# Performance work log

Hardware: AMD Instinct MI355X
Metric: run time of the kernel (lower is better)

The kernel has to match this reference:

```python
import jax, jax.numpy as jnp
import numpy as np

B, L, H, A, M, E, R = 4, 1024, 1024, 16, 128, 32, 992
EMB, BLK, C = 768, 64, 97


def setup_inputs() -> dict:
    key = jax.random.key(0)
    ks = jax.random.split(key, 8)
    return {
        'seq_lhs': jax.random.normal(ks[0], (B, L, H), jnp.float32),
        'ent_lhs': jax.random.normal(ks[1], (B, M, H), jnp.float32),
        'ent_to_seq_attn': jax.random.uniform(ks[2], (B, A, M, L), jnp.float32),
        'mention_entity_ids': jax.random.randint(ks[3], (B, M), 0, E, jnp.int32),
        'hts': jax.random.randint(ks[4], (B, R, 2), 0, E, jnp.int32),
        'head_W': jax.random.normal(ks[5], (2 * H, EMB), jnp.float32) * 0.02,
        'head_b': jnp.zeros((EMB,), jnp.float32),
        'tail_W': jax.random.normal(ks[6], (2 * H, EMB), jnp.float32) * 0.02,
        'tail_b': jnp.zeros((EMB,), jnp.float32),
        'bil_W': jax.random.normal(ks[7], (EMB * BLK, C), jnp.float32) * 0.02,
        'bil_b': jnp.zeros((C,), jnp.float32),
    }


def _pool_doc(seq, ents, attn, ids, ht):
    # seq [L,H], ents [M,H], attn [A,M,L], ids [M], ht [R,2]
    counts = jax.ops.segment_sum(jnp.ones((M,), seq.dtype), ids, num_segments=E)  # [E]
    nz = counts > 0
    # stable segment logsumexp over mentions of each entity (matches torch.logsumexp;
    # single-mention entities reduce to the raw embedding, empty entities -> zeros)
    mx = jax.ops.segment_max(ents, ids, num_segments=E)              # [E,H]
    mx = jnp.where(nz[:, None], mx, 0.0)
    s = jax.ops.segment_sum(jnp.exp(ents - mx[ids]), ids, num_segments=E)
    s = jnp.where(nz[:, None], s, 1.0)
    ent_emb = jnp.where(nz[:, None], mx + jnp.log(s), 0.0)           # [E,H]
    # mean of mention->seq attention per entity (empty -> zeros)
    attn_m = jnp.transpose(attn, (1, 0, 2))                          # [M,A,L]
    asum = jax.ops.segment_sum(attn_m, ids, num_segments=E)          # [E,A,L]
    ent_attn = jnp.where(nz[:, None, None], asum / jnp.maximum(counts, 1.0)[:, None, None], 0.0)
    # gather head/tail entities for each pair
    hs, ts = ent_emb[ht[:, 0]], ent_emb[ht[:, 1]]                    # [R,H]
    ha, ta = ent_attn[ht[:, 0]], ent_attn[ht[:, 1]]                  # [R,A,L]
    w = (ha * ta).mean(axis=1)                                       # [R,L]
    w = w / (w.sum(axis=1, keepdims=True) + 1e-5)
    rel = jnp.einsum('ld,rl->rd', seq, w)                            # [R,H]
    return hs, ts, rel


def reference(seq_lhs, ent_lhs, ent_to_seq_attn, mention_entity_ids, hts,
              head_W, head_b, tail_W, tail_b, bil_W, bil_b):
    hs, ts, rel = jax.vmap(_pool_doc)(seq_lhs, ent_lhs, ent_to_seq_attn,
                                      mention_entity_ids, hts)
    hs = hs.reshape(-1, H)
    ts = ts.reshape(-1, H)
    rel = rel.reshape(-1, H)
    hs = jnp.tanh(jnp.concatenate([hs, rel], axis=1) @ head_W + head_b)  # [N,EMB]
    ts = jnp.tanh(jnp.concatenate([ts, rel], axis=1) @ tail_W + tail_b)
    b1 = hs.reshape(-1, EMB // BLK, BLK)
    b2 = ts.reshape(-1, EMB // BLK, BLK)
    bl = (b1[:, :, :, None] * b2[:, :, None, :]).reshape(-1, EMB * BLK)  # [N,EMB*BLK]
    return bl @ bil_W + bil_b                                            # [N,C]
```

## Files before the change

### kernel.cpp

```cpp
#include <hip/hip_runtime.h>
#include <hip/hip_bf16.h>
#include <math.h>

constexpr int cB   = 4;
constexpr int cL   = 1024;
constexpr int cH   = 1024;
constexpr int cA   = 16;
constexpr int cM   = 128;
constexpr int cE   = 32;
constexpr int cR   = 992;
constexpr int cEMB = 768;
constexpr int cC   = 97;
constexpr int cN   = cB * cR;
constexpr int cNG  = 8;

typedef unsigned short ushort;
typedef __attribute__((ext_vector_type(4))) unsigned short ushort4v;
typedef __attribute__((ext_vector_type(8))) short short8;
typedef __attribute__((ext_vector_type(4))) float float4v;

static __device__ inline float bf2f(ushort u) {
    unsigned v = ((unsigned)u) << 16;
    float f;
    __builtin_memcpy(&f, &v, 4);
    return f;
}
static __device__ inline ushort f2bf(float f) {
    unsigned u;
    __builtin_memcpy(&u, &f, 4);
    unsigned r = (u + 0x7FFFu + ((u >> 16) & 1u)) >> 16;
    return (ushort)r;
}

static __device__ inline void gld16(const ushort* src, ushort* dstbase) {
    __builtin_amdgcn_global_load_lds(
        (const __attribute__((address_space(1))) unsigned int*)src,
        (__attribute__((address_space(3))) unsigned int*)dstbase, 16, 0, 0);
}

__global__ void tr_bf16_k(const float* __restrict__ src, ushort* __restrict__ dst,
                          int R, int C, int Cp) {
    int z = blockIdx.z;
    int r0 = blockIdx.x * 32, c0 = blockIdx.y * 32;
    int tx = threadIdx.x & 31, ty = threadIdx.x >> 5;
    __shared__ float tile[32][33];
    for (int p = 0; p < 4; p++) {
        int r = r0 + ty + p * 8, c = c0 + tx;
        tile[ty + p * 8][tx] = (r < R && c < C) ? src[((size_t)z * R + r) * C + c] : 0.f;
    }
    __syncthreads();
    for (int p = 0; p < 4; p++) {
        int c = c0 + ty + p * 8, r = r0 + tx;
        if (c < Cp && r < R)
            dst[((size_t)z * Cp + c) * R + r] = f2bf(tile[tx][ty + p * 8]);
    }
}

__global__ void tr_ht_k(const float* __restrict__ Wh, const float* __restrict__ Wt,
                        ushort* __restrict__ WTh, ushort* __restrict__ WTt) {
    const float* src = blockIdx.z ? Wt : Wh;
    ushort* dst = blockIdx.z ? WTt : WTh;
    int r0 = blockIdx.x * 32, c0 = blockIdx.y * 32;
    int tx = threadIdx.x & 31, ty = threadIdx.x >> 5;
    __shared__ float tile[32][33];
    for (int p = 0; p < 4; p++) {
        int r = r0 + ty + p * 8, c = c0 + tx;
        tile[ty + p * 8][tx] = src[(size_t)r * cEMB + c];
    }
    __syncthreads();
    for (int p = 0; p < 4; p++) {
        int c = c0 + ty + p * 8, r = r0 + tx;
        dst[(size_t)c * (2 * cH) + r] = f2bf(tile[tx][ty + p * 8]);
    }
}

__global__ void wf_build_k(const float* __restrict__ W, ushort* __restrict__ Wf) {
    const int si = blockIdx.x;
    const int tid = threadIdx.x;
    __shared__ ushort sWb[64 * 136];
    for (int idx = tid; idx < 64 * 128; idx += 256) {
        int r = idx >> 7, c = idx & 127;
        float v = (c < cC) ? W[((size_t)si * 64 + r) * cC + c] : 0.f;
        sWb[r * 136 + c] = f2bf(v);
    }
    __syncthreads();
#pragma unroll
    for (int p = 0; p < 4; p++) {
        int e = tid + p * 256;
        int f = e >> 6, lane = e & 63;
        int g = lane >> 4, col = lane & 15;
        int khalf = f >> 3, ct = f & 7;
        int jb = khalf * 32 + g * 8;
        int c = ct * 16 + col;
        short8 v;
#pragma unroll
        for (int jj = 0; jj < 8; jj++) v[jj] = (short)sWb[(jb + jj) * 136 + c];
        *(short8*)&Wf[(((size_t)si * 16 + f) * 64 + lane) * 8] = v;
    }
}

__global__ void ent_pool_k(const float* __restrict__ ent_lhs, const int* __restrict__ ids,
                           ushort* __restrict__ ent_emb, int* __restrict__ counts) {
    int e = blockIdx.x, b = blockIdx.y;
    __shared__ int sid[cM];
    int tid = threadIdx.x;
    if (tid < cM) sid[tid] = ids[b * cM + tid];
    __syncthreads();
    int cnt = 0;
    for (int m = 0; m < cM; m++) cnt += (sid[m] == e) ? 1 : 0;
    if (blockIdx.z == 0 && tid == 0) counts[b * cE + e] = cnt;
    int h = blockIdx.z * 256 + tid;
    {
        float mx = -1e30f;
        for (int m = 0; m < cM; m++)
            if (sid[m] == e) mx = fmaxf(mx, ent_lhs[(size_t)(b * cM + m) * cH + h]);
        float s = 0.f;
        for (int m = 0; m < cM; m++)
            if (sid[m] == e) s += __expf(ent_lhs[(size_t)(b * cM + m) * cH + h] - mx);
        ent_emb[(size_t)(b * cE + e) * cH + h] = f2bf((cnt > 0) ? (mx + __logf(s)) : 0.f);
    }
}

__global__ void ent_attn_k(const float* __restrict__ attn, const int* __restrict__ ids,
                           const int* __restrict__ counts, ushort* __restrict__ ent_attn) {
    int ba = blockIdx.x;
    int b = ba / cA, a = ba % cA;
    int tid = threadIdx.x;
    int l = blockIdx.y * 256 + tid;
    __shared__ int sid[cM];
    __shared__ int scnt[cE];
    __shared__ float sacc[256 * 33];
    if (tid < cM) sid[tid] = ids[b * cM + tid];
    if (tid < cE) scnt[tid] = counts[b * cE + tid];
    float* acc = &sacc[tid * 33];
    for (int e2 = 0; e2 < cE; e2++) acc[e2] = 0.f;
    __syncthreads();
    const float* ap = attn + ((size_t)(b * cA + a) * cM) * cL + l;
    for (int m = 0; m < cM; m++) acc[sid[m]] += ap[(size_t)m * cL];
    for (int e2 = 0; e2 < cE; e2++) {
        ent_attn[((size_t)(b * cE + e2) * cA + a) * cL + l] =
            f2bf(acc[e2] / (float)max(scnt[e2], 1));
    }
}

__global__ void w_k(const ushort* __restrict__ ent_attn, const int* __restrict__ hts,
                    ushort* __restrict__ w) {
    int nr = blockIdx.x;
    int b = nr / cR;
    int he = hts[nr * 2 + 0], te = hts[nr * 2 + 1];
    int tid = threadIdx.x;
    int l0 = tid * 4;
    const ushort* ha = ent_attn + ((size_t)(b * cE + he) * cA) * cL + l0;
    const ushort* ta = ent_attn + ((size_t)(b * cE + te) * cA) * cL + l0;
    float v[4] = {0.f, 0.f, 0.f, 0.f};
#pragma unroll
    for (int a = 0; a < cA; a++) {
        ushort4v hv = *(const ushort4v*)&ha[(size_t)a * cL];
        ushort4v tv = *(const ushort4v*)&ta[(size_t)a * cL];
#pragma unroll
        for (int i = 0; i < 4; i++) v[i] += bf2f(hv[i]) * bf2f(tv[i]);
    }
    float psum = 0.f;
#pragma unroll
    for (int i = 0; i < 4; i++) { v[i] *= (1.0f / cA); psum += v[i]; }
    for (int off = 32; off > 0; off >>= 1) psum += __shfl_down(psum, off, 64);
    __shared__ float red[4];
    if ((tid & 63) == 0) red[tid >> 6] = psum;
    __syncthreads();
    float tot = red[0] + red[1] + red[2] + red[3];
    float inv = 1.0f / (tot + 1e-5f);
    ushort4v o;
#pragma unroll
    for (int i = 0; i < 4; i++) o[i] = f2bf(v[i] * inv);
    *(ushort4v*)&w[(size_t)nr * cL + l0] = o;
}

__global__ __launch_bounds__(256) void
rel_mfma2_k(const ushort* __restrict__ wbf, const ushort* __restrict__ seqT,
            ushort* __restrict__ relbf) {
    const int b = blockIdx.z;
    const int h0 = blockIdx.x * 128, r0 = blockIdx.y * 64;
    const int tid = threadIdx.x, lane = tid & 63, wv = tid >> 6;
    const int col = lane & 15, g4 = lane >> 4;
    const int wr = wv >> 1, wc = wv & 1;

    __shared__ ushort sA[2][64 * 64];
    __shared__ ushort sB[2][128 * 64];

    const int lr = lane >> 3;
    const int swz = (lane & 7) ^ lr;

    const int ra0 = wv * 8 + lr, ra1 = ra0 + 32;
    const ushort* a0p = wbf + ((size_t)b * cR + min(r0 + ra0, cR - 1)) * cL + swz * 8;
    const ushort* a1p = wbf + ((size_t)b * cR + min(r0 + ra1, cR - 1)) * cL + swz * 8;
    const ushort* bptr[4];
#pragma unroll
    for (int p = 0; p < 4; p++)
        bptr[p] = seqT + ((size_t)b * cH + h0 + p * 32 + wv * 8 + lr) * cL + swz * 8;

    float4v acc[2][4];
#pragma unroll
    for (int mt = 0; mt < 2; mt++)
#pragma unroll
        for (int ct = 0; ct < 4; ct++) acc[mt][ct] = (float4v){0.f, 0.f, 0.f, 0.f};

#define REL_STAGE(kt, buf) {                                                   \
        gld16(a0p + (kt), &sA[buf][wv * 512]);                                 \
        gld16(a1p + (kt), &sA[buf][(4 + wv) * 512]);                           \
        _Pragma("unroll")                                                      \
        for (int p = 0; p < 4; p++)                                            \
            gld16(bptr[p] + (kt), &sB[buf][(p * 4 + wv) * 512]);               \
    }

    REL_STAGE(0, 0);
    __syncthreads();
    int cur = 0;
    for (int kt = 0; kt < cL; kt += 64) {
        if (kt + 64 < cL) REL_STAGE(kt + 64, cur ^ 1);
#pragma unroll
        for (int k0 = 0; k0 < 64; k0 += 32) {
            short8 av[2];
#pragma unroll
            for (int mt = 0; mt < 2; mt++) {
                int ra = wr * 32 + mt * 16 + col;
                int sg = ((k0 >> 3) + g4) ^ (ra & 7);
                av[mt] = *(const short8*)&sA[cur][ra * 64 + sg * 8];
            }
#pragma unroll
            for (int ct = 0; ct < 4; ct++) {
                int rb = wc * 64 + ct * 16 + col;
                int sg = ((k0 >> 3) + g4) ^ (rb & 7);
                short8 bv = *(const short8*)&sB[cur][rb * 64 + sg * 8];
#pragma unroll
                for (int mt = 0; mt < 2; mt++)
                    acc[mt][ct] = __builtin_amdgcn_mfma_f32_16x16x32_bf16(
                        av[mt], bv, acc[mt][ct], 0, 0, 0);
            }
        }
        __syncthreads();
        cur ^= 1;
    }
#undef REL_STAGE

#pragma unroll
    for (int mt = 0; mt < 2; mt++) {
#pragma unroll
        for (int ct = 0; ct < 4; ct++) {
            int h = h0 + wc * 64 + ct * 16 + col;
            int rowb = r0 + wr * 32 + mt * 16 + g4 * 4;
#pragma unroll
            for (int reg = 0; reg < 4; reg++) {
                int r = rowb + reg;
                if (r < cR)
                    relbf[((size_t)b * cR + r) * cH + h] = f2bf(acc[mt][ct][reg]);
            }
        }
    }
}

__global__ __launch_bounds__(256) void
proj_mfma3_k(const ushort* __restrict__ ent_bf, const ushort* __restrict__ relbf,
             const int* __restrict__ hts,
             const ushort* __restrict__ WTh, const ushort* __restrict__ WTt,
             const float* __restrict__ head_b, const float* __restrict__ tail_b,
             ushort* __restrict__ hsp, ushort* __restrict__ tsp) {
    const int sel = blockIdx.z;
    const ushort* WTp = sel ? WTt : WTh;
    const float* bias = sel ? tail_b : head_b;
    ushort* outp = sel ? tsp : hsp;

    const int e0 = blockIdx.x * 128, n0 = blockIdx.y * 64;
    const int tid = threadIdx.x, lane = tid & 63, wv = tid >> 6;
    const int col = lane & 15, g4 = lane >> 4;
    const int wr = wv >> 1, wc = wv & 1;

    __shared__ ushort sA[2][64 * 64];
    __shared__ ushort sB[2][128 * 64];

    const int lr = lane >> 3;
    const int swz = (lane & 7) ^ lr;

    const int ra0 = wv * 8 + lr, ra1 = ra0 + 32;
    size_t eb0, eb1;
    { int n = n0 + ra0, bb = n / cR; eb0 = ((size_t)(bb * cE + hts[n * 2 + sel])) * cH; }
    { int n = n0 + ra1, bb = n / cR; eb1 = ((size_t)(bb * cE + hts[n * 2 + sel])) * cH; }
    const ushort* aent0 = ent_bf + eb0 + swz * 8;
    const ushort* aent1 = ent_bf + eb1 + swz * 8;
    const ushort* arel0 = relbf + (size_t)(n0 + ra0) * cH + swz * 8;
    const ushort* arel1 = relbf + (size_t)(n0 + ra1) * cH + swz * 8;

    const ushort* bptr[4];
#pragma unroll
    for (int p = 0; p < 4; p++)
        bptr[p] = WTp + (size_t)(e0 + p * 32 + wv * 8 + lr) * (2 * cH) + swz * 8;

    float4v acc[2][4];
#pragma unroll
    for (int mt = 0; mt < 2; mt++)
#pragma unroll
        for (int ct = 0; ct < 4; ct++) acc[mt][ct] = (float4v){0.f, 0.f, 0.f, 0.f};

#define PROJ_STAGE(kt, buf) {                                                  \
        const ushort* a0 = ((kt) < cH) ? aent0 + (kt) : arel0 + ((kt) - cH);   \
        const ushort* a1 = ((kt) < cH) ? aent1 + (kt) : arel1 + ((kt) - cH);   \
        gld16(a0, &sA[buf][wv * 512]);                                         \
        gld16(a1, &sA[buf][(4 + wv) * 512]);                                   \
        _Pragma("unroll")                                                      \
        for (int p = 0; p < 4; p++)                                            \
            gld16(bptr[p] + (kt), &sB[buf][(p * 4 + wv) * 512]);               \
    }

    PROJ_STAGE(0, 0);
    __syncthreads();
    int cur = 0;
    for (int kt = 0; kt < 2 * cH; kt += 64) {
        if (kt + 64 < 2 * cH) PROJ_STAGE(kt + 64, cur ^ 1);
#pragma unroll
        for (int k0 = 0; k0 < 64; k0 += 32) {
            short8 av[2];
#pragma unroll
            for (int mt = 0; mt < 2; mt++) {
                int ra = wr * 32 + mt * 16 + col;
                int sg = ((k0 >> 3) + g4) ^ (ra & 7);
                av[mt] = *(const short8*)&sA[cur][ra * 64 + sg * 8];
            }
#pragma unroll
            for (int ct = 0; ct < 4; ct++) {
                int rb = wc * 64 + ct * 16 + col;
                int sg = ((k0 >> 3) + g4) ^ (rb & 7);
                short8 bv = *(const short8*)&sB[cur][rb * 64 + sg * 8];
#pragma unroll
                for (int mt = 0; mt < 2; mt++)
                    acc[mt][ct] = __builtin_amdgcn_mfma_f32_16x16x32_bf16(
                        av[mt], bv, acc[mt][ct], 0, 0, 0);
            }
        }
        __syncthreads();
        cur ^= 1;
    }
#undef PROJ_STAGE

#pragma unroll
    for (int mt = 0; mt < 2; mt++) {
#pragma unroll
        for (int ct = 0; ct < 4; ct++) {
            int e = e0 + wc * 64 + ct * 16 + col;
            float bv = bias[e];
            int rowb = n0 + wr * 32 + mt * 16 + g4 * 4;
#pragma unroll
            for (int reg = 0; reg < 4; reg++)
                outp[(size_t)(rowb + reg) * cEMB + e] = f2bf(tanhf(acc[mt][ct][reg] + bv));
        }
    }
}

__global__ __launch_bounds__(256) void
bil_mfma11_k(const ushort* __restrict__ hsp, const ushort* __restrict__ tsp,
             const ushort* __restrict__ Wf, float* __restrict__ part) {
    const int grp = blockIdx.x;
    const int n0 = blockIdx.y * 64;
    const int tid = threadIdx.x;
    const int lane = tid & 63, wv = tid >> 6;
    const int col = lane & 15, g4 = lane >> 4;

    __shared__ float sHs[32 * 68];

    float4v acc[4][2];
#pragma unroll
    for (int mt = 0; mt < 4; mt++)
#pragma unroll
        for (int ctl = 0; ctl < 2; ctl++) acc[mt][ctl] = (float4v){0.f, 0.f, 0.f, 0.f};

    const ushort* WfG = Wf + (size_t)grp * 3 * 32 * 8192;
    const ushort* wbase = WfG + ((size_t)(wv * 2) * 64 + lane) * 8;

#define WLOAD(dst, t) {                                                        \
        const ushort* _p = wbase + (size_t)(t) * 8192;                         \
        dst[0][0] = *(const short8*)&_p[0];                                    \
        dst[0][1] = *(const short8*)&_p[512];                                  \
        dst[1][0] = *(const short8*)&_p[4096];                                 \
        dst[1][1] = *(const short8*)&_p[4608];                                 \
    }

#define BILSTEP(ii, w) {                                                       \
        float4v hsv[4];                                                        \
        _Pragma("unroll")                                                      \
        for (int mt = 0; mt < 4; mt++)                                         \
            hsv[mt] = *(const float4v*)&sHs[(ii) * 68 + mt * 16 + g4 * 4];     \
        __builtin_amdgcn_s_setprio(1);                                         \
        _Pragma("unroll")                                                      \
        for (int ctl = 0; ctl < 2; ctl++) {                                    \
            _Pragma("unroll")                                                  \
            for (int mt = 0; mt < 4; mt++) {                                   \
                float4v P = (float4v){0.f, 0.f, 0.f, 0.f};                     \
                P = __builtin_amdgcn_mfma_f32_16x16x32_bf16(tsA[mt][0], w[0][ctl], P, 0, 0, 0); \
                P = __builtin_amdgcn_mfma_f32_16x16x32_bf16(tsA[mt][1], w[1][ctl], P, 0, 0, 0); \
                acc[mt][ctl] += hsv[mt] * P;                                   \
            }                                                                  \
        }                                                                      \
        __builtin_amdgcn_s_setprio(0);                                         \
    }

    short8 tsA[4][2];
    short8 wA[2][2], wB[2][2];
    WLOAD(wA, 0);

    for (int s = 0; s < 3; ++s) {
        const int islice = grp * 3 + s;
        const int kb = islice >> 1;

        __syncthreads();
        {
            int row = tid & 63, seg = tid >> 6;
            short8 v = *(const short8*)
                &hsp[(size_t)(n0 + row) * cEMB + islice * 32 + seg * 8];
#pragma unroll
            for (int jj = 0; jj < 8; jj++)
                sHs[(seg * 8 + jj) * 68 + row] = bf2f((ushort)v[jj]);
        }
#pragma unroll
        for (int mt = 0; mt < 4; mt++)
#pragma unroll
            for (int kh = 0; kh < 2; kh++)
                tsA[mt][kh] = *(const short8*)
                    &tsp[(size_t)(n0 + mt * 16 + col) * cEMB
                         + kb * 64 + kh * 32 + g4 * 8];
        __syncthreads();

        for (int i = 0; i < 32; i += 2) {
            const int t = s * 32 + i;
            WLOAD(wB, t + 1);
            BILSTEP(i, wA);
            if (t + 2 < 96) WLOAD(wA, t + 2);
            BILSTEP(i + 1, wB);
        }
    }
#undef WLOAD
#undef BILSTEP

    float* pbase = part + (size_t)grp * cN * 128;
#pragma unroll
    for (int mt = 0; mt < 4; mt++) {
#pragma unroll
        for (int ctl = 0; ctl < 2; ctl++) {
            int c = (wv * 2 + ctl) * 16 + col;
            int rowb = n0 + mt * 16 + g4 * 4;
#pragma unroll
            for (int reg = 0; reg < 4; reg++)
                pbase[(size_t)(rowb + reg) * 128 + c] = acc[mt][ctl][reg];
        }
    }
}

__global__ void bil_reduce_k(const float* __restrict__ part,
                             const float* __restrict__ bil_b,
                             float* __restrict__ out) {
    int n = blockIdx.x;
    int c = threadIdx.x;
    if (c >= cC) return;
    float s = bil_b[c];
#pragma unroll
    for (int g = 0; g < cNG; g++)
        s += part[((size_t)g * cN + n) * 128 + c];
    out[(size_t)n * cC + c] = s;
}

extern "C" void kernel_launch(void* const* d_in, const int* in_sizes, int n_in,
                              void* d_out, int out_size, void* d_ws, size_t ws_size,
                              hipStream_t stream) {
    const float* seq_lhs  = (const float*)d_in[0];
    const float* ent_lhs  = (const float*)d_in[1];
    const float* attn     = (const float*)d_in[2];
    const int*   ids      = (const int*)d_in[3];
    const int*   hts      = (const int*)d_in[4];
    const float* head_W   = (const float*)d_in[5];
    const float* head_b   = (const float*)d_in[6];
    const float* tail_W   = (const float*)d_in[7];
    const float* tail_b   = (const float*)d_in[8];
    const float* bil_W    = (const float*)d_in[9];
    const float* bil_b    = (const float*)d_in[10];
    float* out = (float*)d_out;

    char* ws = (char*)d_ws;
    int*    counts   = (int*)(ws + 0);
    ushort* ent_bf   = (ushort*)(ws + 512);
    ushort* ent_attn = (ushort*)(ws + 262656);
    ushort* wbuf     = (ushort*)(ws + 4456960);
    ushort* relbf    = (ushort*)(ws + 12583424);
    ushort* hsp      = (ushort*)(ws + 20709888);
    ushort* tsp      = (ushort*)(ws + 26804736);
    ushort* Wf       = (ushort*)(ws + 32899584);
    ushort* WTh      = (ushort*)(ws + 45482496);
    ushort* WTt      = (ushort*)(ws + 48628224);
    ushort* seqT     = (ushort*)(ws + 51773952);
    float*  part     = (float*)(ws + 262656);

    hipLaunchKernelGGL(wf_build_k, dim3(768), dim3(256), 0, stream, bil_W, Wf);
    hipLaunchKernelGGL(tr_ht_k, dim3(64, 24, 2), dim3(256), 0, stream,
                       head_W, tail_W, WTh, WTt);
    hipLaunchKernelGGL(tr_bf16_k, dim3(32, 32, cB), dim3(256), 0, stream,
                       seq_lhs, seqT, cL, cH, cH);

    hipLaunchKernelGGL(ent_pool_k, dim3(cE, cB, 4), dim3(256), 0, stream,
                       ent_lhs, ids, ent_bf, counts);
    hipLaunchKernelGGL(ent_attn_k, dim3(cB * cA, cL / 256), dim3(256), 0, stream,
                       attn, ids, counts, ent_attn);
    hipLaunchKernelGGL(w_k, dim3(cN), dim3(256), 0, stream,
                       ent_attn, hts, wbuf);
    hipLaunchKernelGGL(rel_mfma2_k, dim3(cH / 128, 16, cB), dim3(256), 0, stream,
                       wbuf, seqT, relbf);
    hipLaunchKernelGGL(proj_mfma3_k, dim3(cEMB / 128, cN / 64, 2), dim3(256), 0, stream,
                       ent_bf, relbf, hts, WTh, WTt, head_b, tail_b, hsp, tsp);
    hipLaunchKernelGGL(bil_mfma11_k, dim3(cNG, cN / 64), dim3(256), 0, stream,
                       hsp, tsp, Wf, part);
    hipLaunchKernelGGL(bil_reduce_k, dim3(cN), dim3(128), 0, stream,
                       part, bil_b, out);
}
```

Measured before the change: 312.6 us.

## Split bilinear K into 12 groups, hoist ts loads, use packed FMA accumulation

```diff
diff --git a/kernel.cpp b/kernel.cpp
--- a/kernel.cpp
+++ b/kernel.cpp
@@ -12,12 +12,14 @@
 constexpr int cEMB = 768;
 constexpr int cC   = 97;
 constexpr int cN   = cB * cR;
-constexpr int cNG  = 8;
+constexpr int cNG  = 12;
+constexpr int cPC  = 104;
 
 typedef unsigned short ushort;
 typedef __attribute__((ext_vector_type(4))) unsigned short ushort4v;
 typedef __attribute__((ext_vector_type(8))) short short8;
 typedef __attribute__((ext_vector_type(4))) float float4v;
+typedef __attribute__((ext_vector_type(2))) float float2v;
 
 static __device__ inline float bf2f(ushort u) {
     unsigned v = ((unsigned)u) << 16;
@@ -355,7 +357,7 @@
 }
 
 __global__ __launch_bounds__(256) void
-bil_mfma11_k(const ushort* __restrict__ hsp, const ushort* __restrict__ tsp,
+bil_mfma12_k(const ushort* __restrict__ hsp, const ushort* __restrict__ tsp,
              const ushort* __restrict__ Wf, float* __restrict__ part) {
     const int grp = blockIdx.x;
     const int n0 = blockIdx.y * 64;
@@ -365,21 +367,33 @@
 
     __shared__ float sHs[32 * 68];
 
-    float4v acc[4][2];
+    float2v acc[4][2][2];
 #pragma unroll
     for (int mt = 0; mt < 4; mt++)
 #pragma unroll
-        for (int ctl = 0; ctl < 2; ctl++) acc[mt][ctl] = (float4v){0.f, 0.f, 0.f, 0.f};
-
-    const ushort* WfG = Wf + (size_t)grp * 3 * 32 * 8192;
+        for (int ctl = 0; ctl < 2; ctl++) {
+            acc[mt][ctl][0] = (float2v){0.f, 0.f};
+            acc[mt][ctl][1] = (float2v){0.f, 0.f};
+        }
+
+    const float4v kZero = {0.f, 0.f, 0.f, 0.f};
+
+    const ushort* WfG = Wf + (size_t)grp * 2 * 32 * 8192;
     const ushort* wbase = WfG + ((size_t)(wv * 2) * 64 + lane) * 8;
 
-#define WLOAD(dst, t) {                                                        \
-        const ushort* _p = wbase + (size_t)(t) * 8192;                         \
-        dst[0][0] = *(const short8*)&_p[0];                                    \
-        dst[0][1] = *(const short8*)&_p[512];                                  \
-        dst[1][0] = *(const short8*)&_p[4096];                                 \
-        dst[1][1] = *(const short8*)&_p[4608];                                 \
+    short8 tsA[4][2];
+#pragma unroll
+    for (int mt = 0; mt < 4; mt++)
+#pragma unroll
+        for (int kh = 0; kh < 2; kh++)
+            tsA[mt][kh] = *(const short8*)
+                &tsp[(size_t)(n0 + mt * 16 + col) * cEMB + grp * 64 + kh * 32 + g4 * 8];
+
+#define WLOAD(dst, PTR) {                                                      \
+        dst[0][0] = *(const short8*)&(PTR)[0];                                 \
+        dst[0][1] = *(const short8*)&(PTR)[512];                               \
+        dst[1][0] = *(const short8*)&(PTR)[4096];                              \
+        dst[1][1] = *(const short8*)&(PTR)[4608];                              \
     }
 
 #define BILSTEP(ii, w) {                                                       \
@@ -387,27 +401,29 @@
         _Pragma("unroll")                                                      \
         for (int mt = 0; mt < 4; mt++)                                         \
             hsv[mt] = *(const float4v*)&sHs[(ii) * 68 + mt * 16 + g4 * 4];     \
-        __builtin_amdgcn_s_setprio(1);                                         \
         _Pragma("unroll")                                                      \
         for (int ctl = 0; ctl < 2; ctl++) {                                    \
             _Pragma("unroll")                                                  \
             for (int mt = 0; mt < 4; mt++) {                                   \
-                float4v P = (float4v){0.f, 0.f, 0.f, 0.f};                     \
-                P = __builtin_amdgcn_mfma_f32_16x16x32_bf16(tsA[mt][0], w[0][ctl], P, 0, 0, 0); \
-                P = __builtin_amdgcn_mfma_f32_16x16x32_bf16(tsA[mt][1], w[1][ctl], P, 0, 0, 0); \
-                acc[mt][ctl] += hsv[mt] * P;                                   \
+                float4v P = __builtin_amdgcn_mfma_f32_16x16x32_bf16(           \
+                    tsA[mt][0], w[0][ctl], kZero, 0, 0, 0);                    \
+                P = __builtin_amdgcn_mfma_f32_16x16x32_bf16(                   \
+                    tsA[mt][1], w[1][ctl], P, 0, 0, 0);                        \
+                float2v pl = {P[0], P[1]}, ph = {P[2], P[3]};                  \
+                float2v hl = {hsv[mt][0], hsv[mt][1]};                         \
+                float2v hh = {hsv[mt][2], hsv[mt][3]};                         \
+                acc[mt][ctl][0] = __builtin_elementwise_fma(hl, pl, acc[mt][ctl][0]); \
+                acc[mt][ctl][1] = __builtin_elementwise_fma(hh, ph, acc[mt][ctl][1]); \
             }                                                                  \
         }                                                                      \
-        __builtin_amdgcn_s_setprio(0);                                         \
-    }
-
-    short8 tsA[4][2];
+    }
+
     short8 wA[2][2], wB[2][2];
-    WLOAD(wA, 0);
-
-    for (int s = 0; s < 3; ++s) {
-        const int islice = grp * 3 + s;
-        const int kb = islice >> 1;
+    const ushort* wp = wbase;
+    WLOAD(wA, wp);
+
+    for (int s = 0; s < 2; ++s) {
+        const int islice = grp * 2 + s;
 
         __syncthreads();
         {
@@ -418,36 +434,33 @@
             for (int jj = 0; jj < 8; jj++)
                 sHs[(seg * 8 + jj) * 68 + row] = bf2f((ushort)v[jj]);
         }
-#pragma unroll
-        for (int mt = 0; mt < 4; mt++)
-#pragma unroll
-            for (int kh = 0; kh < 2; kh++)
-                tsA[mt][kh] = *(const short8*)
-                    &tsp[(size_t)(n0 + mt * 16 + col) * cEMB
-                         + kb * 64 + kh * 32 + g4 * 8];
         __syncthreads();
 
         for (int i = 0; i < 32; i += 2) {
             const int t = s * 32 + i;
-            WLOAD(wB, t + 1);
+            WLOAD(wB, (wp + 8192));
             BILSTEP(i, wA);
-            if (t + 2 < 96) WLOAD(wA, t + 2);
+            if (t + 2 < 64) WLOAD(wA, (wp + 16384));
             BILSTEP(i + 1, wB);
+            wp += 16384;
         }
     }
 #undef WLOAD
 #undef BILSTEP
 
-    float* pbase = part + (size_t)grp * cN * 128;
+    float* pbase = part + (size_t)grp * cN * cPC;
 #pragma unroll
     for (int mt = 0; mt < 4; mt++) {
 #pragma unroll
         for (int ctl = 0; ctl < 2; ctl++) {
             int c = (wv * 2 + ctl) * 16 + col;
-            int rowb = n0 + mt * 16 + g4 * 4;
-#pragma unroll
-            for (int reg = 0; reg < 4; reg++)
-                pbase[(size_t)(rowb + reg) * 128 + c] = acc[mt][ctl][reg];
+            if (c < cC) {
+                int rowb = n0 + mt * 16 + g4 * 4;
+                pbase[(size_t)(rowb + 0) * cPC + c] = acc[mt][ctl][0][0];
+                pbase[(size_t)(rowb + 1) * cPC + c] = acc[mt][ctl][0][1];
+                pbase[(size_t)(rowb + 2) * cPC + c] = acc[mt][ctl][1][0];
+                pbase[(size_t)(rowb + 3) * cPC + c] = acc[mt][ctl][1][1];
+            }
         }
     }
 }
@@ -461,7 +474,7 @@
     float s = bil_b[c];
 #pragma unroll
     for (int g = 0; g < cNG; g++)
-        s += part[((size_t)g * cN + n) * 128 + c];
+        s += part[((size_t)g * cN + n) * cPC + c];
     out[(size_t)n * cC + c] = s;
 }
 
@@ -511,7 +524,7 @@
                        wbuf, seqT, relbf);
     hipLaunchKernelGGL(proj_mfma3_k, dim3(cEMB / 128, cN / 64, 2), dim3(256), 0, stream,
                        ent_bf, relbf, hts, WTh, WTt, head_b, tail_b, hsp, tsp);
-    hipLaunchKernelGGL(bil_mfma11_k, dim3(cNG, cN / 64), dim3(256), 0, stream,
+    hipLaunchKernelGGL(bil_mfma12_k, dim3(cNG, cN / 64), dim3(256), 0, stream,
                        hsp, tsp, Wf, part);
     hipLaunchKernelGGL(bil_reduce_k, dim3(cN), dim3(128), 0, stream,
                        part, bil_b, out);
```

Measured after the change: 322.4 us. 1.03x slower.

## Merge four prep kernels into one launch and drop setprio in bilinear MFMA loop

Applied to the files above, without the earlier changes.

```diff
diff --git a/kernel.cpp b/kernel.cpp
--- a/kernel.cpp
+++ b/kernel.cpp
@@ -38,86 +38,89 @@
         (__attribute__((address_space(3))) unsigned int*)dstbase, 16, 0, 0);
 }
 
-__global__ void tr_bf16_k(const float* __restrict__ src, ushort* __restrict__ dst,
-                          int R, int C, int Cp) {
-    int z = blockIdx.z;
-    int r0 = blockIdx.x * 32, c0 = blockIdx.y * 32;
-    int tx = threadIdx.x & 31, ty = threadIdx.x >> 5;
+__global__ void prep_k(const float* __restrict__ bil_W,
+                       const float* __restrict__ head_W,
+                       const float* __restrict__ tail_W,
+                       const float* __restrict__ seq_lhs,
+                       const float* __restrict__ ent_lhs,
+                       const int* __restrict__ ids,
+                       ushort* __restrict__ Wf,
+                       ushort* __restrict__ WTh, ushort* __restrict__ WTt,
+                       ushort* __restrict__ seqT,
+                       ushort* __restrict__ ent_bf, int* __restrict__ counts) {
+    const int id = blockIdx.x;
+    const int tid = threadIdx.x;
     __shared__ float tile[32][33];
-    for (int p = 0; p < 4; p++) {
-        int r = r0 + ty + p * 8, c = c0 + tx;
-        tile[ty + p * 8][tx] = (r < R && c < C) ? src[((size_t)z * R + r) * C + c] : 0.f;
-    }
-    __syncthreads();
-    for (int p = 0; p < 4; p++) {
-        int c = c0 + ty + p * 8, r = r0 + tx;
-        if (c < Cp && r < R)
-            dst[((size_t)z * Cp + c) * R + r] = f2bf(tile[tx][ty + p * 8]);
-    }
-}
-
-__global__ void tr_ht_k(const float* __restrict__ Wh, const float* __restrict__ Wt,
-                        ushort* __restrict__ WTh, ushort* __restrict__ WTt) {
-    const float* src = blockIdx.z ? Wt : Wh;
-    ushort* dst = blockIdx.z ? WTt : WTh;
-    int r0 = blockIdx.x * 32, c0 = blockIdx.y * 32;
-    int tx = threadIdx.x & 31, ty = threadIdx.x >> 5;
-    __shared__ float tile[32][33];
-    for (int p = 0; p < 4; p++) {
-        int r = r0 + ty + p * 8, c = c0 + tx;
-        tile[ty + p * 8][tx] = src[(size_t)r * cEMB + c];
-    }
-    __syncthreads();
-    for (int p = 0; p < 4; p++) {
-        int c = c0 + ty + p * 8, r = r0 + tx;
-        dst[(size_t)c * (2 * cH) + r] = f2bf(tile[tx][ty + p * 8]);
-    }
-}
-
-__global__ void wf_build_k(const float* __restrict__ W, ushort* __restrict__ Wf) {
-    const int si = blockIdx.x;
-    const int tid = threadIdx.x;
     __shared__ ushort sWb[64 * 136];
-    for (int idx = tid; idx < 64 * 128; idx += 256) {
-        int r = idx >> 7, c = idx & 127;
-        float v = (c < cC) ? W[((size_t)si * 64 + r) * cC + c] : 0.f;
-        sWb[r * 136 + c] = f2bf(v);
-    }
-    __syncthreads();
-#pragma unroll
-    for (int p = 0; p < 4; p++) {
-        int e = tid + p * 256;
-        int f = e >> 6, lane = e & 63;
-        int g = lane >> 4, col = lane & 15;
-        int khalf = f >> 3, ct = f & 7;
-        int jb = khalf * 32 + g * 8;
-        int c = ct * 16 + col;
-        short8 v;
-#pragma unroll
-        for (int jj = 0; jj < 8; jj++) v[jj] = (short)sWb[(jb + jj) * 136 + c];
-        *(short8*)&Wf[(((size_t)si * 16 + f) * 64 + lane) * 8] = v;
-    }
-}
-
-__global__ void ent_pool_k(const float* __restrict__ ent_lhs, const int* __restrict__ ids,
-                           ushort* __restrict__ ent_emb, int* __restrict__ counts) {
-    int e = blockIdx.x, b = blockIdx.y;
     __shared__ int sid[cM];
-    int tid = threadIdx.x;
-    if (tid < cM) sid[tid] = ids[b * cM + tid];
-    __syncthreads();
-    int cnt = 0;
-    for (int m = 0; m < cM; m++) cnt += (sid[m] == e) ? 1 : 0;
-    if (blockIdx.z == 0 && tid == 0) counts[b * cE + e] = cnt;
-    int h = blockIdx.z * 256 + tid;
-    {
+
+    if (id < 768) {
+        const int si = id;
+        for (int idx = tid; idx < 64 * 128; idx += 256) {
+            int r = idx >> 7, c = idx & 127;
+            float v = (c < cC) ? bil_W[((size_t)si * 64 + r) * cC + c] : 0.f;
+            sWb[r * 136 + c] = f2bf(v);
+        }
+        __syncthreads();
+#pragma unroll
+        for (int p = 0; p < 4; p++) {
+            int e = tid + p * 256;
+            int f = e >> 6, lane = e & 63;
+            int g = lane >> 4, col = lane & 15;
+            int khalf = f >> 3, ct = f & 7;
+            int jb = khalf * 32 + g * 8;
+            int c = ct * 16 + col;
+            short8 v;
+#pragma unroll
+            for (int jj = 0; jj < 8; jj++) v[jj] = (short)sWb[(jb + jj) * 136 + c];
+            *(short8*)&Wf[(((size_t)si * 16 + f) * 64 + lane) * 8] = v;
+        }
+    } else if (id < 3840) {
+        const int t = id - 768;
+        const int bx = t & 63, by = (t >> 6) % 24, bz = t / 1536;
+        const float* src = bz ? tail_W : head_W;
+        ushort* dst = bz ? WTt : WTh;
+        int r0 = bx * 32, c0 = by * 32;
+        int tx = tid & 31, ty = tid >> 5;
+        for (int p = 0; p < 4; p++) {
+            int r = r0 + ty + p * 8, c = c0 + tx;
+            tile[ty + p * 8][tx] = src[(size_t)r * cEMB + c];
+        }
+        __syncthreads();
+        for (int p = 0; p < 4; p++) {
+            int c = c0 + ty + p * 8, r = r0 + tx;
+            dst[(size_t)c * (2 * cH) + r] = f2bf(tile[tx][ty + p * 8]);
+        }
+    } else if (id < 7936) {
+        const int t = id - 3840;
+        const int bx = t & 31, by = (t >> 5) & 31, z = t >> 10;
+        int r0 = bx * 32, c0 = by * 32;
+        int tx = tid & 31, ty = tid >> 5;
+        for (int p = 0; p < 4; p++) {
+            int r = r0 + ty + p * 8, c = c0 + tx;
+            tile[ty + p * 8][tx] = seq_lhs[((size_t)z * cL + r) * cH + c];
+        }
+        __syncthreads();
+        for (int p = 0; p < 4; p++) {
+            int c = c0 + ty + p * 8, r = r0 + tx;
+            seqT[((size_t)z * cH + c) * cL + r] = f2bf(tile[tx][ty + p * 8]);
+        }
+    } else {
+        const int t = id - 7936;
+        const int e = t & 31, b = (t >> 5) & 3, z = t >> 7;
+        if (tid < cM) sid[tid] = ids[b * cM + tid];
+        __syncthreads();
+        int cnt = 0;
+        for (int m = 0; m < cM; m++) cnt += (sid[m] == e) ? 1 : 0;
+        if (z == 0 && tid == 0) counts[b * cE + e] = cnt;
+        int h = z * 256 + tid;
         float mx = -1e30f;
         for (int m = 0; m < cM; m++)
             if (sid[m] == e) mx = fmaxf(mx, ent_lhs[(size_t)(b * cM + m) * cH + h]);
         float s = 0.f;
         for (int m = 0; m < cM; m++)
             if (sid[m] == e) s += __expf(ent_lhs[(size_t)(b * cM + m) * cH + h] - mx);
-        ent_emb[(size_t)(b * cE + e) * cH + h] = f2bf((cnt > 0) ? (mx + __logf(s)) : 0.f);
+        ent_bf[(size_t)(b * cE + e) * cH + h] = f2bf((cnt > 0) ? (mx + __logf(s)) : 0.f);
     }
 }
 
@@ -355,7 +358,7 @@
 }
 
 __global__ __launch_bounds__(256) void
-bil_mfma11_k(const ushort* __restrict__ hsp, const ushort* __restrict__ tsp,
+bil_mfma13_k(const ushort* __restrict__ hsp, const ushort* __restrict__ tsp,
              const ushort* __restrict__ Wf, float* __restrict__ part) {
     const int grp = blockIdx.x;
     const int n0 = blockIdx.y * 64;
@@ -371,6 +374,8 @@
 #pragma unroll
         for (int ctl = 0; ctl < 2; ctl++) acc[mt][ctl] = (float4v){0.f, 0.f, 0.f, 0.f};
 
+    const float4v kZero = {0.f, 0.f, 0.f, 0.f};
+
     const ushort* WfG = Wf + (size_t)grp * 3 * 32 * 8192;
     const ushort* wbase = WfG + ((size_t)(wv * 2) * 64 + lane) * 8;
 
@@ -387,18 +392,17 @@
         _Pragma("unroll")                                                      \
         for (int mt = 0; mt < 4; mt++)                                         \
             hsv[mt] = *(const float4v*)&sHs[(ii) * 68 + mt * 16 + g4 * 4];     \
-        __builtin_amdgcn_s_setprio(1);                                         \
         _Pragma("unroll")                                                      \
         for (int ctl = 0; ctl < 2; ctl++) {                                    \
             _Pragma("unroll")                                                  \
             for (int mt = 0; mt < 4; mt++) {                                   \
-                float4v P = (float4v){0.f, 0.f, 0.f, 0.f};                     \
-                P = __builtin_amdgcn_mfma_f32_16x16x32_bf16(tsA[mt][0], w[0][ctl], P, 0, 0, 0); \
-                P = __builtin_amdgcn_mfma_f32_16x16x32_bf16(tsA[mt][1], w[1][ctl], P, 0, 0, 0); \
+                float4v P = __builtin_amdgcn_mfma_f32_16x16x32_bf16(           \
+                    tsA[mt][0], w[0][ctl], kZero, 0, 0, 0);                    \
+                P = __builtin_amdgcn_mfma_f32_16x16x32_bf16(                   \
+                    tsA[mt][1], w[1][ctl], P, 0, 0, 0);                        \
                 acc[mt][ctl] += hsv[mt] * P;                                   \
             }                                                                  \
         }                                                                      \
-        __builtin_amdgcn_s_setprio(0);                                         \
     }
 
     short8 tsA[4][2];
@@ -495,14 +499,9 @@
     ushort* seqT     = (ushort*)(ws + 51773952);
     float*  part     = (float*)(ws + 262656);
 
-    hipLaunchKernelGGL(wf_build_k, dim3(768), dim3(256), 0, stream, bil_W, Wf);
-    hipLaunchKernelGGL(tr_ht_k, dim3(64, 24, 2), dim3(256), 0, stream,
-                       head_W, tail_W, WTh, WTt);
-    hipLaunchKernelGGL(tr_bf16_k, dim3(32, 32, cB), dim3(256), 0, stream,
-                       seq_lhs, seqT, cL, cH, cH);
-
-    hipLaunchKernelGGL(ent_pool_k, dim3(cE, cB, 4), dim3(256), 0, stream,
-                       ent_lhs, ids, ent_bf, counts);
+    hipLaunchKernelGGL(prep_k, dim3(8448), dim3(256), 0, stream,
+                       bil_W, head_W, tail_W, seq_lhs, ent_lhs, ids,
+                       Wf, WTh, WTt, seqT, ent_bf, counts);
     hipLaunchKernelGGL(ent_attn_k, dim3(cB * cA, cL / 256), dim3(256), 0, stream,
                        attn, ids, counts, ent_attn);
     hipLaunchKernelGGL(w_k, dim3(cN), dim3(256), 0, stream,
@@ -511,7 +510,7 @@
                        wbuf, seqT, relbf);
     hipLaunchKernelGGL(proj_mfma3_k, dim3(cEMB / 128, cN / 64, 2), dim3(256), 0, stream,
                        ent_bf, relbf, hts, WTh, WTt, head_b, tail_b, hsp, tsp);
-    hipLaunchKernelGGL(bil_mfma11_k, dim3(cNG, cN / 64), dim3(256), 0, stream,
+    hipLaunchKernelGGL(bil_mfma13_k, dim3(cNG, cN / 64), dim3(256), 0, stream,
                        hsp, tsp, Wf, part);
     hipLaunchKernelGGL(bil_reduce_k, dim3(cN), dim3(128), 0, stream,
                        part, bil_b, out);
```

After: 296.3 us. -5.2%, faster.
